# Optimization experiments

Hardware: AMD Instinct MI355X
Metric: run time of the kernel (lower is better)

Reference implementation:

```python
import jax, jax.numpy as jnp
import numpy as np
import math

D = 1024
B, S = 8, 2048


def setup_inputs() -> dict:
    key = jax.random.key(0)
    ks = jax.random.split(key, 8)
    q = jax.random.normal(ks[0], (B, S, D), dtype=jnp.float32)
    k = jax.random.normal(ks[1], (B, S, D), dtype=jnp.float32)
    v1 = jax.random.normal(ks[2], (B, S, D), dtype=jnp.float32)
    mask = jax.random.normal(ks[3], (1, S, S), dtype=jnp.float32)
    # Linear params: torch Linear stores W as [out, in]; init ~ U(-1/sqrt(in), 1/sqrt(in))
    lim = 1.0 / math.sqrt(D)
    W1 = jax.random.uniform(ks[4], (D, D), jnp.float32, -lim, lim)
    b1 = jax.random.uniform(ks[5], (D,), jnp.float32, -lim, lim)
    W2 = jax.random.uniform(ks[6], (D, D), jnp.float32, -lim, lim)
    b2 = jax.random.uniform(ks[7], (D,), jnp.float32, -lim, lim)
    return {"q": q, "k": k, "v1": v1, "mask": mask,
            "W1": W1, "b1": b1, "W2": W2, "b2": b2}


def _proj(x, W1, b1, W2, b2):
    # linear2(linear1(x)); torch Linear: x @ W.T + b
    h = jnp.einsum('bsd,od->bso', x, W1) + b1
    return jnp.einsum('bsd,od->bso', h, W2) + b2


def reference(q, k, v1, mask, W1, b1, W2, b2):
    qp = _proj(q, W1, b1, W2, b2)          # [B,S,D]
    kp = _proj(k, W1, b1, W2, b2)          # [B,S,D]
    scale = 1.0 / math.sqrt(qp.shape[-1])
    qk = jnp.einsum('bqd,bkd->bqk', qp, kp) * scale  # [B,S,S]
    qk = qk + mask                          # broadcast [1,S,S]
    attn = jax.nn.softmax(qk, axis=-1)
    return jnp.einsum('bqk,bkd->bqd', attn, v1)  # [B,S,D]
```

## Files before the change

kernel.cpp:

```cpp
#include <hip/hip_runtime.h>
#include <hip/hip_bf16.h>

typedef __hip_bfloat16 bf16;
typedef __bf16 bf16x8 __attribute__((ext_vector_type(8)));
typedef float f32x4 __attribute__((ext_vector_type(4)));

constexpr int Bn = 8, Sn = 2048, Dn = 1024;
constexpr int BM = 128, BN = 128, BK = 64;

__global__ void cast_f32_bf16_k(const float* __restrict__ x, bf16* __restrict__ y, int n) {
  int i = (blockIdx.x * blockDim.x + threadIdx.x) * 4;
  if (i >= n) return;
  float4 f = *reinterpret_cast<const float4*>(x + i);
  bf16 tmp[4] = {__float2bfloat16(f.x), __float2bfloat16(f.y),
                 __float2bfloat16(f.z), __float2bfloat16(f.w)};
  *reinterpret_cast<short4*>(y + i) = *reinterpret_cast<const short4*>(tmp);
}

__global__ void transpose_cast_k(const float* __restrict__ src0, bf16* __restrict__ dst0,
                                 int R, int C) {
  __shared__ float tile[32][33];
  const int r0 = blockIdx.x * 32, c0 = blockIdx.y * 32, b = blockIdx.z;
  const float* src = src0 + (size_t)b * R * C;
  bf16* dst = dst0 + (size_t)b * C * R;
  const int tx = threadIdx.x & 31, ty = threadIdx.x >> 5;
  #pragma unroll
  for (int i = 0; i < 4; ++i) {
    int r = ty + i * 8;
    tile[r][tx] = src[(size_t)(r0 + r) * C + c0 + tx];
  }
  __syncthreads();
  #pragma unroll
  for (int i = 0; i < 4; ++i) {
    int c = ty + i * 8;
    dst[(size_t)(c0 + c) * R + r0 + tx] = __float2bfloat16(tile[tx][c]);
  }
}

__global__ __launch_bounds__(256)
void bias_compose_k(const float* __restrict__ W2, const float* __restrict__ b1,
                    const float* __restrict__ b2, float* __restrict__ bc) {
  const int row = blockIdx.x;
  const int t = threadIdx.x;
  float4 wv = *reinterpret_cast<const float4*>(W2 + (size_t)row * Dn + t * 4);
  float4 bv = *reinterpret_cast<const float4*>(b1 + t * 4);
  float s = wv.x * bv.x + wv.y * bv.y + wv.z * bv.z + wv.w * bv.w;
  #pragma unroll
  for (int off = 32; off >= 1; off >>= 1) s += __shfl_xor(s, off);
  __shared__ float ssum[4];
  if ((t & 63) == 0) ssum[t >> 6] = s;
  __syncthreads();
  if (t == 0) bc[row] = (ssum[0] + ssum[1]) + (ssum[2] + ssum[3]) + b2[row];
}

__global__ __launch_bounds__(256)
void udot_k(const bf16* __restrict__ wct, const float* __restrict__ bc,
            float* __restrict__ u) {
  const int i = blockIdx.x, t = threadIdx.x;
  short4 wv = *reinterpret_cast<const short4*>(wct + (size_t)i * Dn + t * 4);
  float4 bv = *reinterpret_cast<const float4*>(bc + t * 4);
  float s = __uint_as_float(((unsigned)(unsigned short)wv.x) << 16) * bv.x
          + __uint_as_float(((unsigned)(unsigned short)wv.y) << 16) * bv.y
          + __uint_as_float(((unsigned)(unsigned short)wv.z) << 16) * bv.z
          + __uint_as_float(((unsigned)(unsigned short)wv.w) << 16) * bv.w;
  #pragma unroll
  for (int off = 32; off >= 1; off >>= 1) s += __shfl_xor(s, off);
  __shared__ float ssum[4];
  if ((t & 63) == 0) ssum[t >> 6] = s;
  __syncthreads();
  if (t == 0) u[i] = (ssum[0] + ssum[1]) + (ssum[2] + ssum[3]);
}

__global__ __launch_bounds__(256)
void c0_k(const float* __restrict__ bc, float* __restrict__ c0) {
  const int t = threadIdx.x;
  float4 bv = *reinterpret_cast<const float4*>(bc + t * 4);
  float s = bv.x * bv.x + bv.y * bv.y + bv.z * bv.z + bv.w * bv.w;
  #pragma unroll
  for (int off = 32; off >= 1; off >>= 1) s += __shfl_xor(s, off);
  __shared__ float ssum[4];
  if ((t & 63) == 0) ssum[t >> 6] = s;
  __syncthreads();
  if (t == 0) c0[0] = (ssum[0] + ssum[1]) + (ssum[2] + ssum[3]);
}

__global__ __launch_bounds__(256)
void castdot_k(const float* __restrict__ q, const float* __restrict__ k,
               const float* __restrict__ u, const float* __restrict__ c0,
               bf16* __restrict__ dst, float* __restrict__ qu, float* __restrict__ ku) {
  const int row = blockIdx.x;
  const bool isQ = row < Bn * Sn;
  const float* src = isQ ? q + (size_t)row * Dn : k + (size_t)(row - Bn * Sn) * Dn;
  const int t = threadIdx.x;
  float4 f = *reinterpret_cast<const float4*>(src + t * 4);
  bf16 tmp[4] = {__float2bfloat16(f.x), __float2bfloat16(f.y),
                 __float2bfloat16(f.z), __float2bfloat16(f.w)};
  *reinterpret_cast<short4*>(dst + (size_t)row * Dn + t * 4) =
      *reinterpret_cast<const short4*>(tmp);
  float4 uv = *reinterpret_cast<const float4*>(u + t * 4);
  float s = f.x * uv.x + f.y * uv.y + f.z * uv.z + f.w * uv.w;
  #pragma unroll
  for (int off = 32; off >= 1; off >>= 1) s += __shfl_xor(s, off);
  __shared__ float ssum[4];
  if ((t & 63) == 0) ssum[t >> 6] = s;
  __syncthreads();
  if (t == 0) {
    float tot = (ssum[0] + ssum[1]) + (ssum[2] + ssum[3]);
    if (isQ) qu[row] = tot + c0[0];
    else     ku[row - Bn * Sn] = tot;
  }
}

#define SBAR()  asm volatile("s_barrier" ::: "memory")
#define LGKM0() asm volatile("s_waitcnt lgkmcnt(0)" ::: "memory")
#define VM0()   asm volatile("s_waitcnt vmcnt(0)" ::: "memory")

#define MFMA16() do {                                                         \
    __builtin_amdgcn_s_setprio(1);                                            \
    _Pragma("unroll")                                                         \
    for (int kk = 0; kk < 2; ++kk)                                            \
      _Pragma("unroll")                                                       \
      for (int mi4 = 0; mi4 < 4; ++mi4)                                       \
        _Pragma("unroll")                                                     \
        for (int n2 = 0; n2 < 2; ++n2)                                        \
          acc[mi4][n2] = __builtin_amdgcn_mfma_f32_16x16x32_bf16(             \
              aF[mi4][kk], bF[n2][kk], acc[mi4][n2], 0, 0, 0);                \
    __builtin_amdgcn_s_setprio(0);                                            \
  } while (0)

#define ITER(cur, T) do {                                                     \
    const bool pf = (T) + 1 < NT;                                             \
    if (pf) {                                                                 \
      stage2((1 - (cur)) * 32768,         Abase, (T) + 1);                    \
      stage2((1 - (cur)) * 32768 + 16384, Bbase, (T) + 1);                    \
    }                                                                         \
    _Pragma("unroll")                                                         \
    for (int mi4 = 0; mi4 < 4; ++mi4) {                                       \
      aF[mi4][0] = *reinterpret_cast<const bf16x8*>(pA0 + (cur)*32768 + mi4*2048); \
      aF[mi4][1] = *reinterpret_cast<const bf16x8*>(pA1 + (cur)*32768 + mi4*2048); \
    }                                                                         \
    _Pragma("unroll")                                                         \
    for (int j = 0; j < 2; ++j) {                                             \
      bF[j][0] = *reinterpret_cast<const bf16x8*>(pB0 + (cur)*32768 + j*2048); \
      bF[j][1] = *reinterpret_cast<const bf16x8*>(pB1 + (cur)*32768 + j*2048); \
    }                                                                         \
    LGKM0();                                                                  \
    MFMA16();                                                                 \
    if (pf) VM0();                                                            \
    SBAR();                                                                   \
  } while (0)

template<int EPI>
__global__ __launch_bounds__(512, 4)
void gemm128_k(const bf16* __restrict__ A, const bf16* __restrict__ BT,
               void* __restrict__ Cv, const void* __restrict__ auxv,
               const float* __restrict__ qu, const float* __restrict__ ku,
               int N, int K, long long sAz, long long sBz, long long sCz,
               float scale, int gx, int gy)
{
  __shared__ __align__(128) bf16 sh[2 * 16384];

  const int nwg = (int)gridDim.x;
  const int flat = (int)blockIdx.x;
  const int swz = (flat & 7) * (nwg >> 3) + (flat >> 3);
  const int tn = swz % gx;
  const int rem = swz / gx;
  const int tm = rem % gy;
  const int z  = rem / gy;

  const int t = threadIdx.x, w = t >> 6, lane = t & 63;
  const int wm = w >> 2, wn = w & 3;
  const int fr = lane & 15, kg = lane >> 4;
  const int m0 = tm * BM, n0 = tn * BN;
  const bf16* Abase = A + (size_t)z * sAz + (size_t)m0 * K;
  const bf16* Bbase = BT + (size_t)z * sBz + (size_t)n0 * K;

  f32x4 acc[4][2];
  const f32x4 fz = {0.f, 0.f, 0.f, 0.f};
  #pragma unroll
  for (int i = 0; i < 4; ++i) { acc[i][0] = fz; acc[i][1] = fz; }
  bf16x8 aF[4][2], bF[2][2];

  const char* shB = (const char*)sh;
  const int swzlo = (fr & 3) << 4;
  const int swzhi = (fr & 4) << 4;
  const int aoff0 = (wm * 64 + fr) * 128 + ((kg * 16) ^ swzlo) + swzhi;
  const int boff0 = 16384 + (wn * 32 + fr) * 128 + ((kg * 16) ^ swzlo) + swzhi;
  const char* pA0 = shB + aoff0;
  const char* pA1 = shB + (aoff0 ^ 64);
  const char* pB0 = shB + boff0;
  const char* pB1 = shB + (boff0 ^ 64);

  int gOff[2];
  #pragma unroll
  for (int i = 0; i < 2; ++i) {
    const int slot = i * 512 + w * 64 + lane;
    const int row = slot >> 3;
    const int cb = (slot & 7) ^ (row & 7);
    gOff[i] = row * K + cb * 8;
  }
  auto stage2 = [&](int dstByte, const bf16* gbase, int kt) {
    const bf16* g0 = gbase + (size_t)kt * BK;
    char* db = (char*)sh + dstByte;
    #pragma unroll
    for (int i = 0; i < 2; ++i) {
      __builtin_amdgcn_global_load_lds(
          (__attribute__((address_space(1))) void*)(g0 + gOff[i]),
          (__attribute__((address_space(3))) void*)(db + (i * 512 + w * 64) * 16),
          16, 0, 0);
    }
  };

  const int NT = K / BK;
  stage2(0,     Abase, 0);
  stage2(16384, Bbase, 0);
  VM0();
  SBAR();

  for (int T = 0; T < NT; T += 2) {
    ITER(0, T);
    ITER(1, T + 1);
  }

  const int or0 = kg * 4;
  if constexpr (EPI == 1) {
    bf16* C = (bf16*)Cv + (size_t)z * sCz;
    const float* M = (const float*)auxv;
    const float* quz = qu + (size_t)z * Sn;
    const float* kuz = ku + (size_t)z * Sn;
    #pragma unroll
    for (int mi = 0; mi < 4; ++mi)
      #pragma unroll
      for (int r = 0; r < 4; ++r) {
        const int row = m0 + wm * 64 + mi * 16 + or0 + r;
        const float quv = quz[row];
        #pragma unroll
        for (int nj = 0; nj < 2; ++nj) {
          const int col = n0 + wn * 32 + nj * 16 + fr;
          float v = __expf((acc[mi][nj][r] + quv + kuz[col]) * scale
                           + M[(size_t)row * N + col]);
          C[(size_t)row * N + col] = __float2bfloat16(v);
        }
      }
  } else if constexpr (EPI == 2) {
    float* C = (float*)Cv + (size_t)z * sCz;
    const float* Zb = (const float*)auxv + (size_t)z * Sn;
    #pragma unroll
    for (int mi = 0; mi < 4; ++mi)
      #pragma unroll
      for (int r = 0; r < 4; ++r) {
        const int row = m0 + wm * 64 + mi * 16 + or0 + r;
        const float invZ = 1.0f / Zb[row];
        #pragma unroll
        for (int nj = 0; nj < 2; ++nj) {
          const int col = n0 + wn * 32 + nj * 16 + fr;
          C[(size_t)row * N + col] = acc[mi][nj][r] * invZ;
        }
      }
  } else {
    bf16* C = (bf16*)Cv + (size_t)z * sCz;
    bf16* CT = (EPI == 4) ? (bf16*)const_cast<void*>(auxv) : nullptr;
    #pragma unroll
    for (int mi = 0; mi < 4; ++mi)
      #pragma unroll
      for (int r = 0; r < 4; ++r) {
        const int row = m0 + wm * 64 + mi * 16 + or0 + r;
        #pragma unroll
        for (int nj = 0; nj < 2; ++nj) {
          const int col = n0 + wn * 32 + nj * 16 + fr;
          const bf16 v = __float2bfloat16(acc[mi][nj][r]);
          C[(size_t)row * N + col] = v;
          if constexpr (EPI == 4) CT[(size_t)col * N + row] = v;
        }
      }
  }
}

__global__ __launch_bounds__(256)
void rowsum_k(const bf16* __restrict__ sc, float* __restrict__ Z) {
  const size_t row = blockIdx.x;
  const bf16* p = sc + row * (size_t)Sn;
  const int t = threadIdx.x;
  unsigned short raw[8];
  *reinterpret_cast<int4*>(raw) = *reinterpret_cast<const int4*>(p + t * 8);
  float s = 0.f;
  #pragma unroll
  for (int j = 0; j < 8; ++j) s += __uint_as_float(((unsigned)raw[j]) << 16);
  #pragma unroll
  for (int off = 32; off >= 1; off >>= 1) s += __shfl_xor(s, off);
  __shared__ float ssum[4];
  if ((t & 63) == 0) ssum[t >> 6] = s;
  __syncthreads();
  if (t == 0) Z[row] = (ssum[0] + ssum[1]) + (ssum[2] + ssum[3]);
}

extern "C" void kernel_launch(void* const* d_in, const int* in_sizes, int n_in,
                              void* d_out, int out_size, void* d_ws, size_t ws_size,
                              hipStream_t stream) {
  const float* q    = (const float*)d_in[0];
  const float* k    = (const float*)d_in[1];
  const float* v1   = (const float*)d_in[2];
  const float* mask = (const float*)d_in[3];
  const float* W1   = (const float*)d_in[4];
  const float* b1   = (const float*)d_in[5];
  const float* W2   = (const float*)d_in[6];
  const float* b2   = (const float*)d_in[7];
  float* out = (float*)d_out;

  const size_t nQKD = (size_t)Bn * Sn * Dn;
  const size_t nDD = (size_t)Dn * Dn;
  char* ws = (char*)d_ws;
  bf16* vtb  = (bf16*)ws;
  bf16* qkb  = vtb + nQKD;
  bf16* kgb  = qkb + 2 * nQKD;
  bf16* w1t  = kgb + nQKD;
  bf16* w2b  = w1t + nDD;
  bf16* wcb  = w2b + nDD;
  bf16* wct  = wcb + nDD;
  bf16* gb   = wct + nDD;
  bf16* scb  = gb + nDD;
  float* Zb  = (float*)(scb + (size_t)Bn * Sn * Sn);
  float* qub = Zb + (size_t)Bn * Sn;
  float* kub = qub + (size_t)Bn * Sn;
  float* bcb = kub + (size_t)Bn * Sn;
  float* ub  = bcb + Dn;
  float* c0v = ub + Dn;

  dim3 blk(256);
  cast_f32_bf16_k<<<dim3(Dn * Dn / 4 / 256), blk, 0, stream>>>(W2, w2b, Dn * Dn);
  transpose_cast_k<<<dim3(Dn / 32, Dn / 32, 1), blk, 0, stream>>>(W1, w1t, Dn, Dn);
  transpose_cast_k<<<dim3(Sn / 32, Dn / 32, Bn), blk, 0, stream>>>(v1, vtb, Sn, Dn);
  bias_compose_k<<<dim3(Dn), blk, 0, stream>>>(W2, b1, b2, bcb);

  dim3 gblk(512);
  gemm128_k<4><<<dim3(8 * 8), gblk, 0, stream>>>(
      w2b, w1t, wcb, wct, nullptr, nullptr, Dn, Dn, 0, 0, 0, 1.f, 8, 8);
  gemm128_k<3><<<dim3(8 * 8), gblk, 0, stream>>>(
      wct, wct, gb, nullptr, nullptr, nullptr, Dn, Dn, 0, 0, 0, 1.f, 8, 8);
  udot_k<<<dim3(Dn), blk, 0, stream>>>(wct, bcb, ub);
  c0_k<<<dim3(1), blk, 0, stream>>>(bcb, c0v);
  castdot_k<<<dim3(2 * Bn * Sn), blk, 0, stream>>>(q, k, ub, c0v, qkb, qub, kub);
  gemm128_k<3><<<dim3(8 * 128), gblk, 0, stream>>>(
      qkb + nQKD, gb, kgb, nullptr, nullptr, nullptr, Dn, Dn, 0, 0, 0, 1.f, 8, 128);
  gemm128_k<1><<<dim3(16 * 16 * Bn), gblk, 0, stream>>>(
      qkb, kgb, scb, mask, qub, kub, Sn, Dn,
      (long long)Sn * Dn, (long long)Sn * Dn, (long long)Sn * Sn, 0.03125f, 16, 16);
  rowsum_k<<<dim3(Bn * Sn), blk, 0, stream>>>(scb, Zb);
  gemm128_k<2><<<dim3(8 * 16 * Bn), gblk, 0, stream>>>(
      scb, vtb, out, Zb, nullptr, nullptr, Dn, Sn,
      (long long)Sn * Sn, (long long)Dn * Sn, (long long)Sn * Dn, 1.f, 8, 16);
}
```

Before: 322.2 us.

## Fuse softmax row-sum into score GEMM epilogue and use 4-wave 128x128 GEMM

The GEMM kernel now runs with 256 threads (4 waves), each wave computing a 64x64 sub-tile instead of 64x32, which doubles per-wave register accumulators and MFMA work per LDS fragment load. The score GEMM epilogue also accumulates per-row exp sums through shared-memory atomics, then does global atomics into Z, which is zeroed by a memset. This removes the separate rowsum kernel and its re-read of the bf16 score matrix. The cost is higher register pressure, fewer waves to hide latency, and row sums taken over unrounded fp32 values rather than the stored bf16 values.

```diff
diff --git a/kernel.cpp b/kernel.cpp
--- a/kernel.cpp
+++ b/kernel.cpp
@@ -115,24 +115,24 @@
 #define LGKM0() asm volatile("s_waitcnt lgkmcnt(0)" ::: "memory")
 #define VM0()   asm volatile("s_waitcnt vmcnt(0)" ::: "memory")
 
-#define MFMA16() do {                                                         \
+#define MFMA32() do {                                                         \
     __builtin_amdgcn_s_setprio(1);                                            \
     _Pragma("unroll")                                                         \
     for (int kk = 0; kk < 2; ++kk)                                            \
       _Pragma("unroll")                                                       \
       for (int mi4 = 0; mi4 < 4; ++mi4)                                       \
         _Pragma("unroll")                                                     \
-        for (int n2 = 0; n2 < 2; ++n2)                                        \
-          acc[mi4][n2] = __builtin_amdgcn_mfma_f32_16x16x32_bf16(             \
-              aF[mi4][kk], bF[n2][kk], acc[mi4][n2], 0, 0, 0);                \
+        for (int nj = 0; nj < 4; ++nj)                                        \
+          acc[mi4][nj] = __builtin_amdgcn_mfma_f32_16x16x32_bf16(             \
+              aF[mi4][kk], bF[nj][kk], acc[mi4][nj], 0, 0, 0);                \
     __builtin_amdgcn_s_setprio(0);                                            \
   } while (0)
 
 #define ITER(cur, T) do {                                                     \
     const bool pf = (T) + 1 < NT;                                             \
     if (pf) {                                                                 \
-      stage2((1 - (cur)) * 32768,         Abase, (T) + 1);                    \
-      stage2((1 - (cur)) * 32768 + 16384, Bbase, (T) + 1);                    \
+      stage4((1 - (cur)) * 32768,         Abase, (T) + 1);                    \
+      stage4((1 - (cur)) * 32768 + 16384, Bbase, (T) + 1);                    \
     }                                                                         \
     _Pragma("unroll")                                                         \
     for (int mi4 = 0; mi4 < 4; ++mi4) {                                       \
@@ -140,25 +140,27 @@
       aF[mi4][1] = *reinterpret_cast<const bf16x8*>(pA1 + (cur)*32768 + mi4*2048); \
     }                                                                         \
     _Pragma("unroll")                                                         \
-    for (int j = 0; j < 2; ++j) {                                             \
-      bF[j][0] = *reinterpret_cast<const bf16x8*>(pB0 + (cur)*32768 + j*2048); \
-      bF[j][1] = *reinterpret_cast<const bf16x8*>(pB1 + (cur)*32768 + j*2048); \
+    for (int nj = 0; nj < 4; ++nj) {                                          \
+      bF[nj][0] = *reinterpret_cast<const bf16x8*>(pB0 + (cur)*32768 + nj*2048); \
+      bF[nj][1] = *reinterpret_cast<const bf16x8*>(pB1 + (cur)*32768 + nj*2048); \
     }                                                                         \
     LGKM0();                                                                  \
-    MFMA16();                                                                 \
+    MFMA32();                                                                 \
     if (pf) VM0();                                                            \
     SBAR();                                                                   \
   } while (0)
 
 template<int EPI>
-__global__ __launch_bounds__(512, 4)
+__global__ __launch_bounds__(256, 2)
 void gemm128_k(const bf16* __restrict__ A, const bf16* __restrict__ BT,
                void* __restrict__ Cv, const void* __restrict__ auxv,
                const float* __restrict__ qu, const float* __restrict__ ku,
+               float* __restrict__ Zout,
                int N, int K, long long sAz, long long sBz, long long sCz,
                float scale, int gx, int gy)
 {
   __shared__ __align__(128) bf16 sh[2 * 16384];
+  __shared__ float zrow[128];
 
   const int nwg = (int)gridDim.x;
   const int flat = (int)blockIdx.x;
@@ -169,51 +171,53 @@
   const int z  = rem / gy;
 
   const int t = threadIdx.x, w = t >> 6, lane = t & 63;
-  const int wm = w >> 2, wn = w & 3;
+  const int wm = w >> 1, wn = w & 1;
   const int fr = lane & 15, kg = lane >> 4;
   const int m0 = tm * BM, n0 = tn * BN;
   const bf16* Abase = A + (size_t)z * sAz + (size_t)m0 * K;
   const bf16* Bbase = BT + (size_t)z * sBz + (size_t)n0 * K;
 
-  f32x4 acc[4][2];
+  f32x4 acc[4][4];
   const f32x4 fz = {0.f, 0.f, 0.f, 0.f};
   #pragma unroll
-  for (int i = 0; i < 4; ++i) { acc[i][0] = fz; acc[i][1] = fz; }
-  bf16x8 aF[4][2], bF[2][2];
+  for (int i = 0; i < 4; ++i)
+    #pragma unroll
+    for (int j = 0; j < 4; ++j) acc[i][j] = fz;
+  bf16x8 aF[4][2], bF[4][2];
 
   const char* shB = (const char*)sh;
   const int swzlo = (fr & 3) << 4;
   const int swzhi = (fr & 4) << 4;
   const int aoff0 = (wm * 64 + fr) * 128 + ((kg * 16) ^ swzlo) + swzhi;
-  const int boff0 = 16384 + (wn * 32 + fr) * 128 + ((kg * 16) ^ swzlo) + swzhi;
+  const int boff0 = 16384 + (wn * 64 + fr) * 128 + ((kg * 16) ^ swzlo) + swzhi;
   const char* pA0 = shB + aoff0;
   const char* pA1 = shB + (aoff0 ^ 64);
   const char* pB0 = shB + boff0;
   const char* pB1 = shB + (boff0 ^ 64);
 
-  int gOff[2];
-  #pragma unroll
-  for (int i = 0; i < 2; ++i) {
-    const int slot = i * 512 + w * 64 + lane;
+  int gOff[4];
+  #pragma unroll
+  for (int i = 0; i < 4; ++i) {
+    const int slot = i * 256 + t;
     const int row = slot >> 3;
     const int cb = (slot & 7) ^ (row & 7);
     gOff[i] = row * K + cb * 8;
   }
-  auto stage2 = [&](int dstByte, const bf16* gbase, int kt) {
+  auto stage4 = [&](int dstByte, const bf16* gbase, int kt) {
     const bf16* g0 = gbase + (size_t)kt * BK;
     char* db = (char*)sh + dstByte;
     #pragma unroll
-    for (int i = 0; i < 2; ++i) {
+    for (int i = 0; i < 4; ++i) {
       __builtin_amdgcn_global_load_lds(
           (__attribute__((address_space(1))) void*)(g0 + gOff[i]),
-          (__attribute__((address_space(3))) void*)(db + (i * 512 + w * 64) * 16),
+          (__attribute__((address_space(3))) void*)(db + (i * 256 + t) * 16),
           16, 0, 0);
     }
   };
 
   const int NT = K / BK;
-  stage2(0,     Abase, 0);
-  stage2(16384, Bbase, 0);
+  stage4(0,     Abase, 0);
+  stage4(16384, Bbase, 0);
   VM0();
   SBAR();
 
@@ -228,20 +232,29 @@
     const float* M = (const float*)auxv;
     const float* quz = qu + (size_t)z * Sn;
     const float* kuz = ku + (size_t)z * Sn;
+    if (t < 128) zrow[t] = 0.f;
+    __syncthreads();
     #pragma unroll
     for (int mi = 0; mi < 4; ++mi)
       #pragma unroll
       for (int r = 0; r < 4; ++r) {
         const int row = m0 + wm * 64 + mi * 16 + or0 + r;
         const float quv = quz[row];
+        float s = 0.f;
         #pragma unroll
-        for (int nj = 0; nj < 2; ++nj) {
-          const int col = n0 + wn * 32 + nj * 16 + fr;
+        for (int nj = 0; nj < 4; ++nj) {
+          const int col = n0 + wn * 64 + nj * 16 + fr;
           float v = __expf((acc[mi][nj][r] + quv + kuz[col]) * scale
                            + M[(size_t)row * N + col]);
           C[(size_t)row * N + col] = __float2bfloat16(v);
+          s += v;
         }
+        #pragma unroll
+        for (int off = 8; off >= 1; off >>= 1) s += __shfl_xor(s, off);
+        if (fr == 0) atomicAdd(&zrow[wm * 64 + mi * 16 + or0 + r], s);
       }
+    __syncthreads();
+    if (t < 128) atomicAdd(&Zout[(size_t)z * Sn + m0 + t], zrow[t]);
   } else if constexpr (EPI == 2) {
     float* C = (float*)Cv + (size_t)z * sCz;
     const float* Zb = (const float*)auxv + (size_t)z * Sn;
@@ -252,8 +265,8 @@
         const int row = m0 + wm * 64 + mi * 16 + or0 + r;
         const float invZ = 1.0f / Zb[row];
         #pragma unroll
-        for (int nj = 0; nj < 2; ++nj) {
-          const int col = n0 + wn * 32 + nj * 16 + fr;
+        for (int nj = 0; nj < 4; ++nj) {
+          const int col = n0 + wn * 64 + nj * 16 + fr;
           C[(size_t)row * N + col] = acc[mi][nj][r] * invZ;
         }
       }
@@ -266,32 +279,14 @@
       for (int r = 0; r < 4; ++r) {
         const int row = m0 + wm * 64 + mi * 16 + or0 + r;
         #pragma unroll
-        for (int nj = 0; nj < 2; ++nj) {
-          const int col = n0 + wn * 32 + nj * 16 + fr;
+        for (int nj = 0; nj < 4; ++nj) {
+          const int col = n0 + wn * 64 + nj * 16 + fr;
           const bf16 v = __float2bfloat16(acc[mi][nj][r]);
           C[(size_t)row * N + col] = v;
           if constexpr (EPI == 4) CT[(size_t)col * N + row] = v;
         }
       }
   }
-}
-
-__global__ __launch_bounds__(256)
-void rowsum_k(const bf16* __restrict__ sc, float* __restrict__ Z) {
-  const size_t row = blockIdx.x;
-  const bf16* p = sc + row * (size_t)Sn;
-  const int t = threadIdx.x;
-  unsigned short raw[8];
-  *reinterpret_cast<int4*>(raw) = *reinterpret_cast<const int4*>(p + t * 8);
-  float s = 0.f;
-  #pragma unroll
-  for (int j = 0; j < 8; ++j) s += __uint_as_float(((unsigned)raw[j]) << 16);
-  #pragma unroll
-  for (int off = 32; off >= 1; off >>= 1) s += __shfl_xor(s, off);
-  __shared__ float ssum[4];
-  if ((t & 63) == 0) ssum[t >> 6] = s;
-  __syncthreads();
-  if (t == 0) Z[row] = (ssum[0] + ssum[1]) + (ssum[2] + ssum[3]);
 }
 
 extern "C" void kernel_launch(void* const* d_in, const int* in_sizes, int n_in,
@@ -327,26 +322,26 @@
   float* c0v = ub + Dn;
 
   dim3 blk(256);
+  hipMemsetAsync(Zb, 0, (size_t)Bn * Sn * sizeof(float), stream);
   cast_f32_bf16_k<<<dim3(Dn * Dn / 4 / 256), blk, 0, stream>>>(W2, w2b, Dn * Dn);
   transpose_cast_k<<<dim3(Dn / 32, Dn / 32, 1), blk, 0, stream>>>(W1, w1t, Dn, Dn);
   transpose_cast_k<<<dim3(Sn / 32, Dn / 32, Bn), blk, 0, stream>>>(v1, vtb, Sn, Dn);
   bias_compose_k<<<dim3(Dn), blk, 0, stream>>>(W2, b1, b2, bcb);
 
-  dim3 gblk(512);
+  dim3 gblk(256);
   gemm128_k<4><<<dim3(8 * 8), gblk, 0, stream>>>(
-      w2b, w1t, wcb, wct, nullptr, nullptr, Dn, Dn, 0, 0, 0, 1.f, 8, 8);
+      w2b, w1t, wcb, wct, nullptr, nullptr, nullptr, Dn, Dn, 0, 0, 0, 1.f, 8, 8);
   gemm128_k<3><<<dim3(8 * 8), gblk, 0, stream>>>(
-      wct, wct, gb, nullptr, nullptr, nullptr, Dn, Dn, 0, 0, 0, 1.f, 8, 8);
+      wct, wct, gb, nullptr, nullptr, nullptr, nullptr, Dn, Dn, 0, 0, 0, 1.f, 8, 8);
   udot_k<<<dim3(Dn), blk, 0, stream>>>(wct, bcb, ub);
   c0_k<<<dim3(1), blk, 0, stream>>>(bcb, c0v);
   castdot_k<<<dim3(2 * Bn * Sn), blk, 0, stream>>>(q, k, ub, c0v, qkb, qub, kub);
   gemm128_k<3><<<dim3(8 * 128), gblk, 0, stream>>>(
-      qkb + nQKD, gb, kgb, nullptr, nullptr, nullptr, Dn, Dn, 0, 0, 0, 1.f, 8, 128);
+      qkb + nQKD, gb, kgb, nullptr, nullptr, nullptr, nullptr, Dn, Dn, 0, 0, 0, 1.f, 8, 128);
   gemm128_k<1><<<dim3(16 * 16 * Bn), gblk, 0, stream>>>(
-      qkb, kgb, scb, mask, qub, kub, Sn, Dn,
+      qkb, kgb, scb, mask, qub, kub, Zb, Sn, Dn,
       (long long)Sn * Dn, (long long)Sn * Dn, (long long)Sn * Sn, 0.03125f, 16, 16);
-  rowsum_k<<<dim3(Bn * Sn), blk, 0, stream>>>(scb, Zb);
   gemm128_k<2><<<dim3(8 * 16 * Bn), gblk, 0, stream>>>(
-      scb, vtb, out, Zb, nullptr, nullptr, Dn, Sn,
+      scb, vtb, out, Zb, nullptr, nullptr, nullptr, Dn, Sn,
       (long long)Sn * Sn, (long long)Dn * Sn, (long long)Sn * Dn, 1.f, 8, 16);
 }
```

After: 348.4 us. 1.08x slower.
